# Kernel tuning notes

Measured on AMD Instinct MI355X. Metric: run time of the kernel, lower is better.

Reference implementation:

```python
import jax, jax.numpy as jnp
import numpy as np

N_QUBITS = 14
N_LAYERS = 6
BATCH = 1024

# ---- gate constructors (PennyLane conventions) ----

def _rx(t):
    # RX(t) = [[cos t/2, -i sin t/2], [-i sin t/2, cos t/2]]
    tc = t.astype(jnp.complex64)
    c = jnp.cos(tc / 2)
    s = jnp.sin(tc / 2)
    return jnp.stack([jnp.stack([c, -1j * s]), jnp.stack([-1j * s, c])])


def _rz(t):
    # RZ(t) = diag(e^{-it/2}, e^{+it/2})
    e = jnp.exp(-1j * t.astype(jnp.complex64) / 2)
    z = jnp.zeros_like(e)
    return jnp.stack([jnp.stack([e, z]), jnp.stack([z, jnp.conj(e)])])


def _ry(t):
    c = jnp.cos(t / 2)
    s = jnp.sin(t / 2)
    return jnp.stack([jnp.stack([c, -s]), jnp.stack([s, c])]).astype(jnp.complex64)


def _rot(phi, theta, omega):
    # PennyLane Rot(phi, theta, omega) = RZ(omega) @ RY(theta) @ RZ(phi)
    return _rz(omega) @ _ry(theta) @ _rz(phi)


# ---- state-vector gate application (state shape: (2,)*n) ----

def _apply_1q(state, gate, w):
    s = jnp.moveaxis(state, w, 0)          # (2, 2^{n-1} view)
    s = jnp.tensordot(gate, s, axes=([1], [0]))
    return jnp.moveaxis(s, 0, w)


def _apply_cnot(state, c, t):
    s = jnp.moveaxis(state, (c, t), (0, 1))  # (2_control, 2_target, ...)
    s = s.at[1].set(s[1, ::-1])              # flip target where control==1
    return jnp.moveaxis(s, (0, 1), (c, t))


def _simulate(xi, weights):
    n = N_QUBITS
    state = jnp.zeros((2,) * n, jnp.complex64).at[(0,) * n].set(1.0)
    # angle encoding: RX(x_i) on wire i
    for w in range(n):
        state = _apply_1q(state, _rx(xi[w]), w)
    # StronglyEntanglingLayers: Rot on every wire, then CNOT ring with range r
    for l in range(N_LAYERS):
        for w in range(n):
            g = _rot(weights[l, w, 0], weights[l, w, 1], weights[l, w, 2])
            state = _apply_1q(state, g, w)
        r = (l % (n - 1)) + 1  # PennyLane default ranges
        for w in range(n):
            state = _apply_cnot(state, w, (w + r) % n)
    # <Z_0> = P(q0=0) - P(q0=1)
    p = jnp.abs(state.reshape(2, -1)) ** 2
    return jnp.sum(p[0]) - jnp.sum(p[1])


def setup_inputs() -> dict:
    key = jax.random.key(0)
    k1, k2 = jax.random.split(key)
    x = jax.random.normal(k1, (BATCH, N_QUBITS), dtype=jnp.float32)
    weights = 0.01 * jax.random.normal(k2, (N_LAYERS, N_QUBITS, 3), dtype=jnp.float32)
    return {"x": x, "weights": weights}


def reference(x, weights):
    # x: (B, n_qubits) angles -> (B,) expectation values of PauliZ on wire 0
    return jax.vmap(lambda xi: _simulate(xi, weights))(x)
```

## Files before the change

### kernel.cpp

```cpp
#include <hip/hip_runtime.h>
#include <hip/hip_fp16.h>
#include <math.h>

#define NQ 14
#define NL 6
#define NT 512
#define BATCH 1024
#define NGATES (NL * NQ)
#define GINIT 0x111


typedef _Float16 half8 __attribute__((ext_vector_type(8)));
typedef float f32x16 __attribute__((ext_vector_type(16)));

__device__ constexpr int ring_F(int l, int v) {
    int r = (l % 13) + 1;
    for (int w = 0; w < NQ; ++w) {
        int pc = 13 - w, pt = 13 - ((w + r) % NQ);
        v ^= ((v >> pc) & 1) << pt;
    }
    return v;
}

__device__ constexpr int gcorr(int G, int a, int p) {
    int keys = (a & 15) | ((p & 1) << 4);
    int c = 0;
    for (int k = 0; k < 5; ++k) if ((keys >> k) & 1) c ^= (G >> (3 * k)) & 7;
    return c;
}
__device__ constexpr int lam0(int a, int p, int G) {
    int chunk = ((a >> 4) & 31) | (((a >> 12) & 1) << 5) | (((a >> 13) & 1) << 6)
              | ((p & 1) << 7) | ((a & 15) << 8);
    chunk ^= gcorr(G, a, p);
    return ((a >> 9) & 7) | (chunk << 3);
}
__device__ constexpr int lam1(int a, int p) {
    int chunk = (a & 15) | (((a >> 13) & 1) << 4) | (((a >> 7) & 1) << 5)
              | (((a >> 8) & 1) << 6) | ((p & 1) << 7) | (((a >> 12) & 1) << 8)
              | (((a >> 9) & 7) << 9);
    chunk ^= (a >> 9) & 7;
    return ((a >> 4) & 7) | (chunk << 3);
}
__device__ constexpr int lam2(int a, int p) {
    int chunk = ((a >> 9) & 31) | (((a >> 3) & 1) << 5) | ((p & 1) << 6)
              | (((a >> 7) & 3) << 7) | (((a >> 4) & 7) << 9);
    chunk ^= (a >> 4) & 7;
    return (a & 7) | (chunk << 3);
}

__device__ constexpr int vrank5(int v0, int v1, int v2, int v3, int v4, int v5) {
    int vs[6] = {v0, v1, v2, v3, v4, v5};
    int basis[5] = {0, 0, 0, 0, 0};
    int r = 0;
    for (int i = 0; i < 6; ++i) {
        int x = vs[i];
        for (int b = 4; b >= 0; --b) {
            if (((x >> b) & 1) == 0) continue;
            if (basis[b]) { x ^= basis[b]; }
            else { basis[b] = x; ++r; break; }
        }
    }
    return r;
}
__device__ constexpr int scat_rank(int L, int G) {
    return vrank5(
        (lam0(ring_F(L, 1), 0, G) >> 1) & 31,
        (lam0(ring_F(L, 2), 0, G) >> 1) & 31,
        (lam0(ring_F(L, 4), 0, G) >> 1) & 31,
        (lam0(ring_F(L, 8), 0, G) >> 1) & 31,
        (lam0(0, 1, G) >> 1) & 31,
        (lam0(ring_F(L, 1 << 11), 0, G) >> 1) & 31);
}
__device__ constexpr int find_g0(int L) {
    if (scat_rank(L, GINIT) == 5) return GINIT;
    for (int s = 0; s < 15; ++s)
        if (scat_rank(L, GINIT ^ (1 << s)) == 5) return GINIT ^ (1 << s);
    for (int s1 = 0; s1 < 15; ++s1)
        for (int s2 = s1 + 1; s2 < 15; ++s2)
            if (scat_rank(L, GINIT ^ (1 << s1) ^ (1 << s2)) == 5)
                return GINIT ^ (1 << s1) ^ (1 << s2);
    int best = GINIT, br = scat_rank(L, GINIT);
    for (int s = 0; s < 15; ++s) {
        int g = GINIT ^ (1 << s);
        int rr = scat_rank(L, g);
        if (rr > br) { best = g; br = rr; }
    }
    return best;
}
__device__ constexpr int gsrc(int L) { return L < 0 ? GINIT : find_g0(L); }

__global__ void prep_kernel(const float* __restrict__ wts, float* __restrict__ gm) {
    int g = blockIdx.x * blockDim.x + threadIdx.x;
    if (g < NGATES) {
        float phi = wts[g*3+0], th = wts[g*3+1], om = wts[g*3+2];
        float c = cosf(0.5f*th), s = sinf(0.5f*th);
        float a = 0.5f*(phi+om), bb = 0.5f*(phi-om);
        float ca = cosf(a), sa = sinf(a);
        float cb = cosf(bb), sb = sinf(bb);
        gm[g*8+0] = c*ca;  gm[g*8+1] = -c*sa;
        gm[g*8+2] = -s*cb; gm[g*8+3] = -s*sb;
        gm[g*8+4] = s*cb;  gm[g*8+5] = -s*sb;
        gm[g*8+6] = c*ca;  gm[g*8+7] = c*sa;
    }
}

__global__ void prep2_kernel(const float* __restrict__ gm, _Float16* __restrict__ B) {
    int t = blockIdx.x * blockDim.x + threadIdx.x;
    if (t >= NL * 18 * 64) return;
    int lane = t & 63;
    int fi = (t >> 6) % 18;
    int L = t / (18 * 64);
    int a, tt, m;
    if (fi < 8)       { a = 0; tt = fi >> 2;        m = fi & 3; }
    else if (fi < 16) { a = 1; tt = (fi - 8) >> 2;  m = (fi - 8) & 3; }
    else              { a = 2; tt = 0;              m = fi - 16; }
    int h = lane >> 5, c = lane & 31;
    for (int e = 0; e < 8; ++e) {
        int kc, kp, nc, np, nb;
        if (a < 2) { int kr = 16*m + 8*h + e; int nr = 32*tt + c;
                     kc = kr & 31; kp = kr >> 5; nc = nr & 31; np = nr >> 5; nb = 5; }
        else       { kc = 8*h + e; kp = m; nc = c & 15; np = c >> 4; nb = 4; }
        float gr = 1.f, gi = 0.f;
        for (int j = 0; j < nb; ++j) {
            int w = (a == 0) ? (4 - j) : (a == 1) ? (9 - j) : (13 - j);
            const float* mm = gm + (L*NQ + w)*8;
            const float* ent = mm + (((nc >> j) & 1) * 2 + ((kc >> j) & 1)) * 2;
            float er = ent[0], ei = ent[1];
            float ngr = gr*er - gi*ei, ngi = gr*ei + gi*er;
            gr = ngr; gi = ngi;
        }
        float v = (kp == np) ? gr : (kp ? -gi : gi);
        B[((L*18 + fi)*64 + lane)*8 + e] = (_Float16)v;
    }
}

template<int L>
__device__ __forceinline__ void apply0(_Float16* st, const _Float16* B,
                                       int lane, int l31, int h, int w) {
    constexpr int GR = gsrc(L - 1);
    half8 Af[2][4];
    const int rb = lam0(w | (l31 << 4) | (h << 12), 0, GR);
    #pragma unroll
    for (int ss = 0; ss < 2; ++ss)
        #pragma unroll
        for (int m = 0; m < 4; ++m)
            Af[ss][m] = *(const half8*)(st + (rb ^ lam0((ss << 3) | ((m & 1) << 13), m >> 1, GR)));
    __syncthreads();
    half8 Bf[8];
    #pragma unroll
    for (int f = 0; f < 8; ++f)
        Bf[f] = *(const half8*)(B + ((L*18 + f)*64 + lane)*8);
    const int wb = lam1(w | (h << 6) | (l31 << 9), 0);
    #pragma unroll
    for (int ss = 0; ss < 2; ++ss)
        #pragma unroll
        for (int t = 0; t < 2; ++t) {
            f32x16 acc;
            #pragma unroll
            for (int j = 0; j < 16; ++j) acc[j] = 0.f;
            #pragma unroll
            for (int m = 0; m < 4; ++m)
                acc = __builtin_amdgcn_mfma_f32_32x32x16_f16(Af[ss][m], Bf[t*4+m], acc, 0, 0, 0);
            #pragma unroll
            for (int q = 0; q < 4; ++q) {
                uint2 wv;
                wv.x = __builtin_bit_cast(unsigned, __builtin_amdgcn_cvt_pkrtz(acc[4*q+0], acc[4*q+1]));
                wv.y = __builtin_bit_cast(unsigned, __builtin_amdgcn_cvt_pkrtz(acc[4*q+2], acc[4*q+3]));
                *(uint2*)(st + (wb ^ lam1((ss << 3) | ((q & 1) << 7) | ((q >> 1) << 8), t))) = wv;
            }
        }
    __syncthreads();
}

template<int L>
__device__ __forceinline__ void apply1(_Float16* st, const _Float16* B,
                                       int lane, int l31, int h, int w) {
    half8 Af[2][4];
    const int rb = lam1((l31 & 15) | (h << 7) | (w << 9) | (((l31 >> 4) & 1) << 13), 0);
    #pragma unroll
    for (int ss = 0; ss < 2; ++ss)
        #pragma unroll
        for (int m = 0; m < 4; ++m)
            Af[ss][m] = *(const half8*)(st + (rb ^ lam1((ss << 12) | ((m & 1) << 8), m >> 1)));
    __syncthreads();
    half8 Bf[8];
    #pragma unroll
    for (int f = 0; f < 8; ++f)
        Bf[f] = *(const half8*)(B + ((L*18 + 8 + f)*64 + lane)*8);
    const int wb = lam2((h << 2) | (l31 << 4) | (w << 9), 0);
    #pragma unroll
    for (int ss = 0; ss < 2; ++ss)
        #pragma unroll
        for (int t = 0; t < 2; ++t) {
            f32x16 acc;
            #pragma unroll
            for (int j = 0; j < 16; ++j) acc[j] = 0.f;
            #pragma unroll
            for (int m = 0; m < 4; ++m)
                acc = __builtin_amdgcn_mfma_f32_32x32x16_f16(Af[ss][m], Bf[t*4+m], acc, 0, 0, 0);
            #pragma unroll
            for (int q = 0; q < 4; ++q) {
                uint2 wv;
                wv.x = __builtin_bit_cast(unsigned, __builtin_amdgcn_cvt_pkrtz(acc[4*q+0], acc[4*q+1]));
                wv.y = __builtin_bit_cast(unsigned, __builtin_amdgcn_cvt_pkrtz(acc[4*q+2], acc[4*q+3]));
                *(uint2*)(st + (wb ^ lam2((ss << 12) | ((q & 1) << 3) | ((q >> 1) << 13), t))) = wv;
            }
        }
    __syncthreads();
}

template<int L>
__device__ __forceinline__ void apply2(_Float16* st, const _Float16* B,
                                       int lane, int l31, int h, int w) {
    constexpr int GW = find_g0(L);
    half8 Af[4][2];
    const int rb = lam2((h << 3) | (w << 4) | (l31 << 9), 0);
    #pragma unroll
    for (int ss = 0; ss < 4; ++ss)
        #pragma unroll
        for (int m = 0; m < 2; ++m)
            Af[ss][m] = *(const half8*)(st + (rb ^ lam2(ss << 7, m)));
    __syncthreads();
    half8 Bf[2];
    #pragma unroll
    for (int f = 0; f < 2; ++f)
        Bf[f] = *(const half8*)(B + ((L*18 + 16 + f)*64 + lane)*8);
    constexpr int C0 = lam0(ring_F(L, 1), 0, GW);
    constexpr int C1 = lam0(ring_F(L, 2), 0, GW);
    constexpr int C2 = lam0(ring_F(L, 4), 0, GW);
    constexpr int C3 = lam0(ring_F(L, 8), 0, GW);
    constexpr int CP = lam0(0, 1, GW);
    constexpr int CH = lam0(ring_F(L, 1 << 11), 0, GW);
    constexpr int CW0 = lam0(ring_F(L, 1 << 4), 0, GW);
    constexpr int CW1 = lam0(ring_F(L, 1 << 5), 0, GW);
    constexpr int CW2 = lam0(ring_F(L, 1 << 6), 0, GW);
    constexpr int CS0 = lam0(ring_F(L, 1 << 7), 0, GW);
    constexpr int CS1 = lam0(ring_F(L, 1 << 8), 0, GW);
    constexpr int E9  = lam0(ring_F(L, 1 << 9), 0, GW);
    constexpr int E10 = lam0(ring_F(L, 1 << 10), 0, GW);
    constexpr int E12 = lam0(ring_F(L, 1 << 12), 0, GW);
    constexpr int E13 = lam0(ring_F(L, 1 << 13), 0, GW);
    int wb = ((l31 & 1) ? C0 : 0) ^ ((l31 & 2) ? C1 : 0) ^ ((l31 & 4) ? C2 : 0)
           ^ ((l31 & 8) ? C3 : 0) ^ ((l31 & 16) ? CP : 0) ^ (h ? CH : 0)
           ^ ((w & 1) ? CW0 : 0) ^ ((w & 2) ? CW1 : 0) ^ ((w & 4) ? CW2 : 0);
    #pragma unroll
    for (int ss = 0; ss < 4; ++ss) {
        f32x16 acc;
        #pragma unroll
        for (int j = 0; j < 16; ++j) acc[j] = 0.f;
        acc = __builtin_amdgcn_mfma_f32_32x32x16_f16(Af[ss][0], Bf[0], acc, 0, 0, 0);
        acc = __builtin_amdgcn_mfma_f32_32x32x16_f16(Af[ss][1], Bf[1], acc, 0, 0, 0);
        const int ws_ = wb ^ ((ss & 1) ? CS0 : 0) ^ ((ss & 2) ? CS1 : 0);
        #pragma unroll
        for (int r = 0; r < 16; ++r) {
            int wa = ws_ ^ ((r & 1) ? E9 : 0) ^ ((r & 2) ? E10 : 0)
                         ^ ((r & 4) ? E12 : 0) ^ ((r & 8) ? E13 : 0);
            st[wa] = (_Float16)acc[r];
        }
    }
    __syncthreads();
}

template<int L>
__device__ __forceinline__ void do_layer(_Float16* st, const _Float16* B,
                                         int lane, int l31, int h, int w) {
    apply0<L>(st, B, lane, l31, h, w);
    apply1<L>(st, B, lane, l31, h, w);
    apply2<L>(st, B, lane, l31, h, w);
    if constexpr (L < NL - 1) do_layer<L+1>(st, B, lane, l31, h, w);
}

__global__ void __launch_bounds__(NT, 4)
qsim_kernel(const float* __restrict__ x, const _Float16* __restrict__ B,
            float* __restrict__ out)
{
    __shared__ _Float16 st[32768];
    const int tid = threadIdx.x;
    const int lane = tid & 63, wid = tid >> 6;
    const int l31 = lane & 31, h = lane >> 5;
    const float* xb = x + blockIdx.x * NQ;

    {
        float cr = 1.f, ci = 0.f;
        #pragma unroll
        for (int bb = 0; bb < 3; ++bb) {
            float s, c; __sincosf(0.5f * xb[13 - bb], &s, &c);
            if ((wid >> bb) & 1) { float nr = s*ci, ni = -s*cr; cr = nr; ci = ni; }
            else                 { cr *= c; ci *= c; }
        }
        {
            float s, c; __sincosf(0.5f * xb[10], &s, &c);
            if (h) { float nr = s*ci, ni = -s*cr; cr = nr; ci = ni; }
            else   { cr *= c; ci *= c; }
        }
        #pragma unroll
        for (int bb = 0; bb < 5; ++bb) {
            float s, c; __sincosf(0.5f * xb[9 - bb], &s, &c);
            if ((l31 >> bb) & 1) { float nr = s*ci, ni = -s*cr; cr = nr; ci = ni; }
            else                 { cr *= c; ci *= c; }
        }
        float es[3], ec[3];
        #pragma unroll
        for (int bb = 0; bb < 3; ++bb) __sincosf(0.5f * xb[4 - bb], &es[bb], &ec[bb]);
        float s1, c1, s0, c0;
        __sincosf(0.5f * xb[1], &s1, &c1);
        __sincosf(0.5f * xb[0], &s0, &c0);
        const int ib = lam0(wid | (h << 3) | (l31 << 4), 0, GINIT);
        #pragma unroll
        for (int j2 = 0; j2 < 4; ++j2) {
            float dr = cr, di = ci;
            if (j2 & 1) { float nr = s1*di, ni = -s1*dr; dr = nr; di = ni; }
            else        { dr *= c1; di *= c1; }
            if (j2 >> 1) { float nr = s0*di, ni = -s0*dr; dr = nr; di = ni; }
            else         { dr *= c0; di *= c0; }
            half8 R, I;
            #pragma unroll
            for (int e = 0; e < 8; ++e) {
                float rr = dr, ii = di;
                #pragma unroll
                for (int bb = 0; bb < 3; ++bb) {
                    if ((e >> bb) & 1) { float nr = es[bb]*ii, ni = -es[bb]*rr; rr = nr; ii = ni; }
                    else               { rr *= ec[bb]; ii *= ec[bb]; }
                }
                R[e] = (_Float16)rr; I[e] = (_Float16)ii;
            }
            int da = ((j2 & 1) << 12) | ((j2 >> 1) << 13);
            *(half8*)(st + (ib ^ lam0(da, 0, GINIT))) = R;
            *(half8*)(st + (ib ^ lam0(da, 1, GINIT))) = I;
        }
    }
    __syncthreads();

    do_layer<0>(st, B, lane, l31, h, wid);

    {
        constexpr int G5 = find_g0(NL - 1);
        const int rb = lam0(wid | (l31 << 4) | (h << 12), 0, G5);
        float acc = 0.f;
        #pragma unroll
        for (int ss = 0; ss < 2; ++ss)
            #pragma unroll
            for (int m0 = 0; m0 < 2; ++m0) {
                half8 re = *(const half8*)(st + (rb ^ lam0((ss << 3) | (m0 << 13), 0, G5)));
                half8 im = *(const half8*)(st + (rb ^ lam0((ss << 3) | (m0 << 13), 1, G5)));
                float s = 0.f;
                #pragma unroll
                for (int e = 0; e < 8; ++e) {
                    float r = (float)re[e], iv = (float)im[e];
                    s += r*r + iv*iv;
                }
                acc += m0 ? -s : s;
            }
        #pragma unroll
        for (int off = 32; off > 0; off >>= 1) acc += __shfl_down(acc, off, 64);
        __syncthreads();
        float* f = (float*)st;
        if ((tid & 63) == 0) f[tid >> 6] = acc;
        __syncthreads();
        if (tid == 0) {
            float s = 0.f;
            #pragma unroll
            for (int w = 0; w < NT/64; ++w) s += f[w];
            out[blockIdx.x] = s;
        }
    }
}

extern "C" void kernel_launch(void* const* d_in, const int* in_sizes, int n_in,
                              void* d_out, int out_size, void* d_ws, size_t ws_size,
                              hipStream_t stream) {
    const float* x = (const float*)d_in[0];
    const float* w = (const float*)d_in[1];
    float* out = (float*)d_out;
    float* gm = (float*)d_ws;
    _Float16* B = (_Float16*)((char*)d_ws + 4096);

    prep_kernel<<<1, 128, 0, stream>>>(w, gm);
    prep2_kernel<<<27, 256, 0, stream>>>(gm, B);
    qsim_kernel<<<BATCH, NT, 0, stream>>>(x, B, out);
}
```

Before: 146.5 us.

## Fuse prep kernels, hoist B-fragment loads, reuse zero accumulator, relax launch bounds

Merges the two weight-preparation kernels into one, so each thread recomputes the needed Rot matrices in registers and one launch plus a global round-trip disappears. Moves the global loads of the B fragments ahead of the shared-memory reads and barrier so their latency overlaps. Passes in a shared zero accumulator for the first MFMA, rewrites the apply2 scatter as a Gray-code XOR walk over addresses, and lowers the launch-bounds occupancy hint from 4 to 2. The trade-off is redundant trig work per prep thread and more register pressure, which may reduce occupancy.

```diff
diff --git a/kernel.cpp b/kernel.cpp
--- a/kernel.cpp
+++ b/kernel.cpp
@@ -89,22 +89,7 @@
 }
 __device__ constexpr int gsrc(int L) { return L < 0 ? GINIT : find_g0(L); }
 
-__global__ void prep_kernel(const float* __restrict__ wts, float* __restrict__ gm) {
-    int g = blockIdx.x * blockDim.x + threadIdx.x;
-    if (g < NGATES) {
-        float phi = wts[g*3+0], th = wts[g*3+1], om = wts[g*3+2];
-        float c = cosf(0.5f*th), s = sinf(0.5f*th);
-        float a = 0.5f*(phi+om), bb = 0.5f*(phi-om);
-        float ca = cosf(a), sa = sinf(a);
-        float cb = cosf(bb), sb = sinf(bb);
-        gm[g*8+0] = c*ca;  gm[g*8+1] = -c*sa;
-        gm[g*8+2] = -s*cb; gm[g*8+3] = -s*sb;
-        gm[g*8+4] = s*cb;  gm[g*8+5] = -s*sb;
-        gm[g*8+6] = c*ca;  gm[g*8+7] = c*sa;
-    }
-}
-
-__global__ void prep2_kernel(const float* __restrict__ gm, _Float16* __restrict__ B) {
+__global__ void prepB_kernel(const float* __restrict__ wts, _Float16* __restrict__ B) {
     int t = blockIdx.x * blockDim.x + threadIdx.x;
     if (t >= NL * 18 * 64) return;
     int lane = t & 63;
@@ -115,19 +100,39 @@
     else if (fi < 16) { a = 1; tt = (fi - 8) >> 2;  m = (fi - 8) & 3; }
     else              { a = 2; tt = 0;              m = fi - 16; }
     int h = lane >> 5, c = lane & 31;
+    const int nb = (a < 2) ? 5 : 4;
+    float gmat[5][8];
+    #pragma unroll
+    for (int j = 0; j < 5; ++j) {
+        if (j < nb) {
+            int w = (a == 0) ? (4 - j) : (a == 1) ? (9 - j) : (13 - j);
+            int g = L * NQ + w;
+            float phi = wts[g*3+0], th = wts[g*3+1], om = wts[g*3+2];
+            float cc = cosf(0.5f*th), sn = sinf(0.5f*th);
+            float aa = 0.5f*(phi+om), bb = 0.5f*(phi-om);
+            float ca = cosf(aa), sa = sinf(aa);
+            float cb = cosf(bb), sb = sinf(bb);
+            gmat[j][0] = cc*ca;  gmat[j][1] = -cc*sa;
+            gmat[j][2] = -sn*cb; gmat[j][3] = -sn*sb;
+            gmat[j][4] = sn*cb;  gmat[j][5] = -sn*sb;
+            gmat[j][6] = cc*ca;  gmat[j][7] = cc*sa;
+        }
+    }
+    #pragma unroll
     for (int e = 0; e < 8; ++e) {
-        int kc, kp, nc, np, nb;
+        int kc, kp, nc, np;
         if (a < 2) { int kr = 16*m + 8*h + e; int nr = 32*tt + c;
-                     kc = kr & 31; kp = kr >> 5; nc = nr & 31; np = nr >> 5; nb = 5; }
-        else       { kc = 8*h + e; kp = m; nc = c & 15; np = c >> 4; nb = 4; }
+                     kc = kr & 31; kp = kr >> 5; nc = nr & 31; np = nr >> 5; }
+        else       { kc = 8*h + e; kp = m; nc = c & 15; np = c >> 4; }
         float gr = 1.f, gi = 0.f;
-        for (int j = 0; j < nb; ++j) {
-            int w = (a == 0) ? (4 - j) : (a == 1) ? (9 - j) : (13 - j);
-            const float* mm = gm + (L*NQ + w)*8;
-            const float* ent = mm + (((nc >> j) & 1) * 2 + ((kc >> j) & 1)) * 2;
-            float er = ent[0], ei = ent[1];
-            float ngr = gr*er - gi*ei, ngi = gr*ei + gi*er;
-            gr = ngr; gi = ngi;
+        #pragma unroll
+        for (int j = 0; j < 5; ++j) {
+            if (j < nb) {
+                const float* ent = &gmat[j][(((nc >> j) & 1) * 2 + ((kc >> j) & 1)) * 2];
+                float er = ent[0], ei = ent[1];
+                float ngr = gr*er - gi*ei, ngi = gr*ei + gi*er;
+                gr = ngr; gi = ngi;
+            }
         }
         float v = (kp == np) ? gr : (kp ? -gi : gi);
         B[((L*18 + fi)*64 + lane)*8 + e] = (_Float16)v;
@@ -136,8 +141,13 @@
 
 template<int L>
 __device__ __forceinline__ void apply0(_Float16* st, const _Float16* B,
-                                       int lane, int l31, int h, int w) {
+                                       int lane, int l31, int h, int w,
+                                       const f32x16 zw) {
     constexpr int GR = gsrc(L - 1);
+    half8 Bf[8];
+    #pragma unroll
+    for (int f = 0; f < 8; ++f)
+        Bf[f] = *(const half8*)(B + ((L*18 + f)*64 + lane)*8);
     half8 Af[2][4];
     const int rb = lam0(w | (l31 << 4) | (h << 12), 0, GR);
     #pragma unroll
@@ -146,20 +156,14 @@
         for (int m = 0; m < 4; ++m)
             Af[ss][m] = *(const half8*)(st + (rb ^ lam0((ss << 3) | ((m & 1) << 13), m >> 1, GR)));
     __syncthreads();
-    half8 Bf[8];
-    #pragma unroll
-    for (int f = 0; f < 8; ++f)
-        Bf[f] = *(const half8*)(B + ((L*18 + f)*64 + lane)*8);
     const int wb = lam1(w | (h << 6) | (l31 << 9), 0);
     #pragma unroll
     for (int ss = 0; ss < 2; ++ss)
         #pragma unroll
         for (int t = 0; t < 2; ++t) {
-            f32x16 acc;
-            #pragma unroll
-            for (int j = 0; j < 16; ++j) acc[j] = 0.f;
-            #pragma unroll
-            for (int m = 0; m < 4; ++m)
+            f32x16 acc = __builtin_amdgcn_mfma_f32_32x32x16_f16(Af[ss][0], Bf[t*4+0], zw, 0, 0, 0);
+            #pragma unroll
+            for (int m = 1; m < 4; ++m)
                 acc = __builtin_amdgcn_mfma_f32_32x32x16_f16(Af[ss][m], Bf[t*4+m], acc, 0, 0, 0);
             #pragma unroll
             for (int q = 0; q < 4; ++q) {
@@ -174,7 +178,12 @@
 
 template<int L>
 __device__ __forceinline__ void apply1(_Float16* st, const _Float16* B,
-                                       int lane, int l31, int h, int w) {
+                                       int lane, int l31, int h, int w,
+                                       const f32x16 zw) {
+    half8 Bf[8];
+    #pragma unroll
+    for (int f = 0; f < 8; ++f)
+        Bf[f] = *(const half8*)(B + ((L*18 + 8 + f)*64 + lane)*8);
     half8 Af[2][4];
     const int rb = lam1((l31 & 15) | (h << 7) | (w << 9) | (((l31 >> 4) & 1) << 13), 0);
     #pragma unroll
@@ -183,20 +192,14 @@
         for (int m = 0; m < 4; ++m)
             Af[ss][m] = *(const half8*)(st + (rb ^ lam1((ss << 12) | ((m & 1) << 8), m >> 1)));
     __syncthreads();
-    half8 Bf[8];
-    #pragma unroll
-    for (int f = 0; f < 8; ++f)
-        Bf[f] = *(const half8*)(B + ((L*18 + 8 + f)*64 + lane)*8);
     const int wb = lam2((h << 2) | (l31 << 4) | (w << 9), 0);
     #pragma unroll
     for (int ss = 0; ss < 2; ++ss)
         #pragma unroll
         for (int t = 0; t < 2; ++t) {
-            f32x16 acc;
-            #pragma unroll
-            for (int j = 0; j < 16; ++j) acc[j] = 0.f;
-            #pragma unroll
-            for (int m = 0; m < 4; ++m)
+            f32x16 acc = __builtin_amdgcn_mfma_f32_32x32x16_f16(Af[ss][0], Bf[t*4+0], zw, 0, 0, 0);
+            #pragma unroll
+            for (int m = 1; m < 4; ++m)
                 acc = __builtin_amdgcn_mfma_f32_32x32x16_f16(Af[ss][m], Bf[t*4+m], acc, 0, 0, 0);
             #pragma unroll
             for (int q = 0; q < 4; ++q) {
@@ -211,8 +214,13 @@
 
 template<int L>
 __device__ __forceinline__ void apply2(_Float16* st, const _Float16* B,
-                                       int lane, int l31, int h, int w) {
+                                       int lane, int l31, int h, int w,
+                                       const f32x16 zw) {
     constexpr int GW = find_g0(L);
+    half8 Bf[2];
+    #pragma unroll
+    for (int f = 0; f < 2; ++f)
+        Bf[f] = *(const half8*)(B + ((L*18 + 16 + f)*64 + lane)*8);
     half8 Af[4][2];
     const int rb = lam2((h << 3) | (w << 4) | (l31 << 9), 0);
     #pragma unroll
@@ -221,10 +229,6 @@
         for (int m = 0; m < 2; ++m)
             Af[ss][m] = *(const half8*)(st + (rb ^ lam2(ss << 7, m)));
     __syncthreads();
-    half8 Bf[2];
-    #pragma unroll
-    for (int f = 0; f < 2; ++f)
-        Bf[f] = *(const half8*)(B + ((L*18 + 16 + f)*64 + lane)*8);
     constexpr int C0 = lam0(ring_F(L, 1), 0, GW);
     constexpr int C1 = lam0(ring_F(L, 2), 0, GW);
     constexpr int C2 = lam0(ring_F(L, 4), 0, GW);
@@ -245,17 +249,17 @@
            ^ ((w & 1) ? CW0 : 0) ^ ((w & 2) ? CW1 : 0) ^ ((w & 4) ? CW2 : 0);
     #pragma unroll
     for (int ss = 0; ss < 4; ++ss) {
-        f32x16 acc;
-        #pragma unroll
-        for (int j = 0; j < 16; ++j) acc[j] = 0.f;
-        acc = __builtin_amdgcn_mfma_f32_32x32x16_f16(Af[ss][0], Bf[0], acc, 0, 0, 0);
+        f32x16 acc = __builtin_amdgcn_mfma_f32_32x32x16_f16(Af[ss][0], Bf[0], zw, 0, 0, 0);
         acc = __builtin_amdgcn_mfma_f32_32x32x16_f16(Af[ss][1], Bf[1], acc, 0, 0, 0);
-        const int ws_ = wb ^ ((ss & 1) ? CS0 : 0) ^ ((ss & 2) ? CS1 : 0);
-        #pragma unroll
-        for (int r = 0; r < 16; ++r) {
-            int wa = ws_ ^ ((r & 1) ? E9 : 0) ^ ((r & 2) ? E10 : 0)
-                         ^ ((r & 4) ? E12 : 0) ^ ((r & 8) ? E13 : 0);
-            st[wa] = (_Float16)acc[r];
+        int wp = wb ^ ((ss & 1) ? CS0 : 0) ^ ((ss & 2) ? CS1 : 0);
+        #pragma unroll
+        for (int j = 0; j < 8; ++j) {
+            int gp = j ^ (j >> 1);
+            st[wp]      = (_Float16)acc[2*gp];
+            st[wp ^ E9] = (_Float16)acc[2*gp + 1];
+            if (j < 7)
+                wp ^= (j == 0 ? E10 : j == 1 ? E12 : j == 2 ? E10 :
+                       j == 3 ? E13 : j == 4 ? E10 : j == 5 ? E12 : E10);
         }
     }
     __syncthreads();
@@ -263,14 +267,15 @@
 
 template<int L>
 __device__ __forceinline__ void do_layer(_Float16* st, const _Float16* B,
-                                         int lane, int l31, int h, int w) {
-    apply0<L>(st, B, lane, l31, h, w);
-    apply1<L>(st, B, lane, l31, h, w);
-    apply2<L>(st, B, lane, l31, h, w);
-    if constexpr (L < NL - 1) do_layer<L+1>(st, B, lane, l31, h, w);
-}
-
-__global__ void __launch_bounds__(NT, 4)
+                                         int lane, int l31, int h, int w,
+                                         const f32x16 zw) {
+    apply0<L>(st, B, lane, l31, h, w, zw);
+    apply1<L>(st, B, lane, l31, h, w, zw);
+    apply2<L>(st, B, lane, l31, h, w, zw);
+    if constexpr (L < NL - 1) do_layer<L+1>(st, B, lane, l31, h, w, zw);
+}
+
+__global__ void __launch_bounds__(NT, 2)
 qsim_kernel(const float* __restrict__ x, const _Float16* __restrict__ B,
             float* __restrict__ out)
 {
@@ -280,6 +285,10 @@
     const int l31 = lane & 31, h = lane >> 5;
     const float* xb = x + blockIdx.x * NQ;
 
+    f32x16 zw;
+    #pragma unroll
+    for (int j = 0; j < 16; ++j) zw[j] = 0.f;
+
     {
         float cr = 1.f, ci = 0.f;
         #pragma unroll
@@ -331,7 +340,7 @@
     }
     __syncthreads();
 
-    do_layer<0>(st, B, lane, l31, h, wid);
+    do_layer<0>(st, B, lane, l31, h, wid, zw);
 
     {
         constexpr int G5 = find_g0(NL - 1);
@@ -372,10 +381,8 @@
     const float* x = (const float*)d_in[0];
     const float* w = (const float*)d_in[1];
     float* out = (float*)d_out;
-    float* gm = (float*)d_ws;
-    _Float16* B = (_Float16*)((char*)d_ws + 4096);
-
-    prep_kernel<<<1, 128, 0, stream>>>(w, gm);
-    prep2_kernel<<<27, 256, 0, stream>>>(gm, B);
+    _Float16* B = (_Float16*)d_ws;
+
+    prepB_kernel<<<27, 256, 0, stream>>>(w, B);
     qsim_kernel<<<BATCH, NT, 0, stream>>>(x, B, out);
 }
```

After: 172.9 us. 1.18x slower.
